# Kernel tuning notes

Hardware: AMD Instinct MI355X
Metric: run time of the kernel (lower is better)

## Reference

```python
import jax, jax.numpy as jnp
import numpy as np

D_MODEL = 768; N_LAYERS = 4; SOC_WINDOW = 10
D_INNER = 2 * D_MODEL; D_STATE = 16; DT_RANK = D_MODEL // 16; D_CONV = 4
EPS = 1e-5
B, T = 4, 1024


def setup_inputs() -> dict:
    key = jax.random.key(0)
    ks = jax.random.split(key, 10)
    w = lambda k, s, sc=0.02: jax.random.normal(k, s, jnp.float32) * sc
    return {
        "x": jax.random.normal(ks[0], (B, T, 2 + SOC_WINDOW), jnp.float32),
        "inp_w": w(ks[1], (D_MODEL, 2 + SOC_WINDOW)),
        "inp_b": jnp.zeros((D_MODEL,), jnp.float32),
        "in_proj_w": w(ks[2], (N_LAYERS, 2 * D_INNER, D_MODEL)),
        "conv_w": w(ks[3], (N_LAYERS, D_INNER, D_CONV), 0.1),
        "conv_b": jnp.zeros((N_LAYERS, D_INNER), jnp.float32),
        "x_proj_w": w(ks[4], (N_LAYERS, DT_RANK + 2 * D_STATE, D_INNER)),
        "dt_proj_w": w(ks[5], (N_LAYERS, D_INNER, DT_RANK), 0.05),
        "dt_proj_b": w(ks[6], (N_LAYERS, D_INNER), 0.5),
        "A_log": jnp.tile(jnp.log(jnp.arange(1.0, D_STATE + 1.0, dtype=jnp.float32)), (N_LAYERS, D_INNER, 1)),
        "D_skip": jnp.ones((N_LAYERS, D_INNER), jnp.float32),
        "out_proj_w": w(ks[7], (N_LAYERS, D_MODEL, D_INNER)),
        "ln_w": jnp.ones((N_LAYERS, D_MODEL), jnp.float32),
        "norm_w": jnp.ones((D_MODEL,), jnp.float32),
        "head_w": w(ks[8], (1, D_MODEL)),
        "head_b": jnp.zeros((1,), jnp.float32),
    }


def _rmsnorm(x, w):
    return x * jax.lax.rsqrt(jnp.mean(x * x, axis=-1, keepdims=True) + EPS) * w


def _mamba_block(x, in_w, cw, cb, xp_w, dtw, dtb, A_log, Dsk, out_w):
    Bsz = x.shape[0]
    xz = jnp.einsum('btd,ed->bte', x, in_w)            # (B,T,2*D_INNER)
    xx, z = jnp.split(xz, 2, axis=-1)
    # causal depthwise conv1d (pad left d_conv-1, truncate to T)
    xc = jax.lax.conv_general_dilated(
        jnp.swapaxes(xx, 1, 2), cw[:, None, :], (1,), [(D_CONV - 1, 0)],
        feature_group_count=D_INNER, dimension_numbers=('NCH', 'OIH', 'NCH'))
    xx = jax.nn.silu(jnp.swapaxes(xc + cb[None, :, None], 1, 2))  # (B,T,D_INNER)
    dbc = jnp.einsum('btd,ed->bte', xx, xp_w)          # (B,T,dt_rank+2*N)
    delta = jax.nn.softplus(jnp.einsum('btr,dr->btd', dbc[..., :DT_RANK], dtw) + dtb)
    Bm = dbc[..., DT_RANK:DT_RANK + D_STATE]           # (B,T,N)
    Cm = dbc[..., DT_RANK + D_STATE:]                  # (B,T,N)
    A = -jnp.exp(A_log)                                # (D_INNER,N)

    def step(h, inp):
        d_t, x_t, b_t, c_t = inp                       # (B,Din),(B,Din),(B,N),(B,N)
        h = jnp.exp(d_t[..., None] * A) * h + (d_t * x_t)[..., None] * b_t[:, None, :]
        return h, jnp.einsum('bdn,bn->bd', h, c_t)

    h0 = jnp.zeros((Bsz, D_INNER, D_STATE), x.dtype)
    _, ys = jax.lax.scan(step, h0, (jnp.moveaxis(delta, 1, 0), jnp.moveaxis(xx, 1, 0),
                                    jnp.moveaxis(Bm, 1, 0), jnp.moveaxis(Cm, 1, 0)))
    y = jnp.moveaxis(ys, 0, 1) + Dsk * xx
    y = y * jax.nn.silu(z)
    return jnp.einsum('bte,de->btd', y, out_w)


def reference(x, inp_w, inp_b, in_proj_w, conv_w, conv_b, x_proj_w, dt_proj_w, dt_proj_b,
              A_log, D_skip, out_proj_w, ln_w, norm_w, head_w, head_b):
    h = jnp.einsum('btf,df->btd', x, inp_w) + inp_b
    for l in range(N_LAYERS):
        h = h + _mamba_block(_rmsnorm(h, ln_w[l]), in_proj_w[l], conv_w[l], conv_b[l],
                             x_proj_w[l], dt_proj_w[l], dt_proj_b[l], A_log[l],
                             D_skip[l], out_proj_w[l])
    h = _rmsnorm(h, norm_w)
    y = jnp.einsum('btd,od->bto', h, head_w) + head_b
    return y[..., 0]
```

## Files before the change

### kernel.cpp

```cpp
#include <hip/hip_runtime.h>
#include <stdint.h>

#define D_MODEL   768
#define D_INNER   1536
#define D_STATE   16
#define DT_RANK   48
#define NB        4
#define TSEQ      1024
#define NTOK      4096
#define EPS       1e-5f
#define CHUNK     32
#define NCHUNK    32
#define XP_N      128

typedef __bf16 bf16;
typedef __bf16 bf16x8 __attribute__((ext_vector_type(8)));
typedef float  floatx4 __attribute__((ext_vector_type(4)));

__device__ __forceinline__ float silu_f(float v)     { return v / (1.f + __expf(-v)); }
__device__ __forceinline__ float softplus_f(float v) { return v > 20.f ? v : __logf(1.f + __expf(v)); }

__device__ __forceinline__ void async_ld16(const void* g, void* l) {
  __builtin_amdgcn_global_load_lds((__attribute__((address_space(1))) uint32_t*)g,
                                   (__attribute__((address_space(3))) uint32_t*)l, 16, 0, 0);
}

__global__ __launch_bounds__(256) void prep_k(const float* __restrict__ win, const float* __restrict__ wout,
                                              bf16* __restrict__ bin, bf16* __restrict__ bout) {
  const int i = blockIdx.x * 256 + threadIdx.x;
  const int NIN = 4 * 3072 * 768;
  if (i < NIN) bin[i] = (bf16)win[i];
  else         bout[i - NIN] = (bf16)wout[i - NIN];
}

__global__ __launch_bounds__(256) void prep_xp_k(const float* __restrict__ w, bf16* __restrict__ wb) {
  const int i = blockIdx.x * 256 + threadIdx.x;
  const int k = i % 1536;
  const int r = (i / 1536) % XP_N;
  const int l = i / (1536 * XP_N);
  wb[i] = (r < 80) ? (bf16)w[((size_t)l * 80 + r) * 1536 + k] : (bf16)0.f;
}

__global__ __launch_bounds__(256) void input_proj_k(const float* __restrict__ x, const float* __restrict__ w,
                                                    const float* __restrict__ bvec, float* __restrict__ h) {
  const int idx = blockIdx.x * 256 + threadIdx.x;
  const int d = idx % D_MODEL;
  const int t = idx / D_MODEL;
  float acc = bvec[d];
  #pragma unroll
  for (int f = 0; f < 12; ++f) acc = fmaf(x[t * 12 + f], w[d * 12 + f], acc);
  h[idx] = acc;
}

__global__ __launch_bounds__(256) void rmsnorm_k(const float* __restrict__ h, const float* __restrict__ lnw,
                                                 bf16* __restrict__ xn) {
  const int t = blockIdx.x;
  const float* __restrict__ hr = h + (size_t)t * D_MODEL;
  float v[3];
  float ss = 0.f;
  #pragma unroll
  for (int i = 0; i < 3; ++i) { v[i] = hr[threadIdx.x + i * 256]; ss = fmaf(v[i], v[i], ss); }
  #pragma unroll
  for (int o = 32; o > 0; o >>= 1) ss += __shfl_down(ss, o, 64);
  __shared__ float red[4];
  if ((threadIdx.x & 63) == 0) red[threadIdx.x >> 6] = ss;
  __syncthreads();
  const float tot = red[0] + red[1] + red[2] + red[3];
  const float rs = rsqrtf(tot / (float)D_MODEL + EPS);
  #pragma unroll
  for (int i = 0; i < 3; ++i) {
    const int d = threadIdx.x + i * 256;
    xn[(size_t)t * D_MODEL + d] = (bf16)(v[i] * rs * lnw[d]);
  }
}

template <int MODE>
__global__ __launch_bounds__(256) void gemm_bt(const bf16* __restrict__ A, const bf16* __restrict__ B,
                                               void* __restrict__ Cv, const int N, const int K, const int kLen) {
  alignas(16) __shared__ bf16 As[128 * 32];
  alignas(16) __shared__ bf16 Bs[128 * 32];
  const int tid = threadIdx.x;
  const int lane = tid & 63;
  const int wid = tid >> 6;
  const int wm = wid & 1, wn = wid >> 1;
  const int m0 = blockIdx.x * 128, n0 = blockIdx.y * 128;
  const int kOff = blockIdx.z * kLen;

  floatx4 acc[4][4];
  #pragma unroll
  for (int i = 0; i < 4; ++i)
    #pragma unroll
    for (int j = 0; j < 4; ++j) acc[i][j] = (floatx4){0.f, 0.f, 0.f, 0.f};

  const int srow = lane >> 2;
  const int skp  = (lane & 3) * 8;
  const int fr = lane & 15;
  const int fk = (lane >> 4) * 8;

  for (int k0 = 0; k0 < kLen; k0 += 32) {
    __syncthreads();
    #pragma unroll
    for (int i = 0; i < 2; ++i) {
      const int seg = wid * 2 + i;
      const int row = seg * 16 + srow;
      async_ld16(A + (size_t)(m0 + row) * K + kOff + k0 + skp, (char*)As + seg * 1024);
      async_ld16(B + (size_t)(n0 + row) * K + kOff + k0 + skp, (char*)Bs + seg * 1024);
    }
    __syncthreads();
    bf16x8 a[4], b[4];
    #pragma unroll
    for (int t = 0; t < 4; ++t) {
      a[t] = *(const bf16x8*)&As[(wm * 64 + t * 16 + fr) * 32 + fk];
      b[t] = *(const bf16x8*)&Bs[(wn * 64 + t * 16 + fr) * 32 + fk];
    }
    #pragma unroll
    for (int i = 0; i < 4; ++i)
      #pragma unroll
      for (int j = 0; j < 4; ++j)
        acc[i][j] = __builtin_amdgcn_mfma_f32_16x16x32_bf16(a[i], b[j], acc[i][j], 0, 0, 0);
  }

  const int quad = lane >> 4, col = lane & 15;
  #pragma unroll
  for (int i = 0; i < 4; ++i)
    #pragma unroll
    for (int j = 0; j < 4; ++j) {
      const int gm0 = m0 + wm * 64 + i * 16 + quad * 4;
      const int gn  = n0 + wn * 64 + j * 16 + col;
      #pragma unroll
      for (int r = 0; r < 4; ++r) {
        const size_t off = (size_t)(gm0 + r) * N + gn;
        const float v = acc[i][j][r];
        if (MODE == 0)      ((float*)Cv)[off] = v;
        else if (MODE == 1) ((bf16*)Cv)[off] = (bf16)v;
        else                atomicAdd(&((float*)Cv)[off], v);
      }
    }
}

__global__ __launch_bounds__(256) void conv_silu_k(const bf16* __restrict__ xz, const float* __restrict__ cw,
                                                   const float* __restrict__ cb, bf16* __restrict__ xxb) {
  const int idx = blockIdx.x * 256 + threadIdx.x;
  const int d = idx % D_INNER;
  const int bt = idx / D_INNER;
  const int t = bt & (TSEQ - 1);
  float acc = cb[d];
  #pragma unroll
  for (int j = 0; j < 4; ++j) {
    const int tt = t - 3 + j;
    if (tt >= 0) acc = fmaf((float)xz[(size_t)(bt - 3 + j) * (2 * D_INNER) + d], cw[d * 4 + j], acc);
  }
  xxb[idx] = (bf16)silu_f(acc);
}

__global__ __launch_bounds__(256) void scan_p1_k(const bf16* __restrict__ xxb, const float* __restrict__ dbc,
                                                 const float* __restrict__ dtw, const float* __restrict__ dtb,
                                                 const float* __restrict__ Alog,
                                                 float* __restrict__ P, float* __restrict__ S) {
  const int c = blockIdx.x;
  const int d = blockIdx.y * 256 + threadIdx.x;
  const int b = blockIdx.z;
  float w[DT_RANK];
  #pragma unroll
  for (int k = 0; k < DT_RANK; k += 4) {
    const float4 t4 = *(const float4*)&dtw[(size_t)d * DT_RANK + k];
    w[k] = t4.x; w[k + 1] = t4.y; w[k + 2] = t4.z; w[k + 3] = t4.w;
  }
  const float bias = dtb[d];
  float A[16], Sv[16], Pv[16];
  #pragma unroll
  for (int n = 0; n < 16; ++n) {
    A[n] = -__expf(Alog[(size_t)d * 16 + n]);
    Sv[n] = 0.f; Pv[n] = 1.f;
  }
  const int bt0 = b * TSEQ + c * CHUNK;
  for (int tt = 0; tt < CHUNK; ++tt) {
    const size_t bt = bt0 + tt;
    const float* __restrict__ db = dbc + bt * XP_N;
    float dacc = bias;
    #pragma unroll
    for (int k = 0; k < DT_RANK; ++k) dacc = fmaf(db[k], w[k], dacc);
    const float du  = softplus_f(dacc);
    const float xv  = (float)xxb[bt * D_INNER + d];
    const float dux = du * xv;
    const float* __restrict__ Bp = db + DT_RANK;
    #pragma unroll
    for (int n = 0; n < 16; ++n) {
      const float e = __expf(du * A[n]);
      Sv[n] = fmaf(e, Sv[n], dux * Bp[n]);
      Pv[n] *= e;
    }
  }
  const size_t base = ((size_t)(b * NCHUNK + c) * 16) * D_INNER + d;
  #pragma unroll
  for (int n = 0; n < 16; ++n) {
    P[base + (size_t)n * D_INNER] = Pv[n];
    S[base + (size_t)n * D_INNER] = Sv[n];
  }
}

__global__ __launch_bounds__(256) void scan_fold_k(const float* __restrict__ P, float* __restrict__ S) {
  const int idx = blockIdx.x * 256 + threadIdx.x;
  const int d = idx % D_INNER;
  const int bn = idx / D_INNER;
  const int n = bn & 15;
  const int b = bn >> 4;
  float H = 0.f;
  #pragma unroll 4
  for (int c = 0; c < NCHUNK; ++c) {
    const size_t off = ((size_t)((b * NCHUNK + c) * 16 + n)) * D_INNER + d;
    const float Pv = P[off], Sv = S[off];
    S[off] = H;
    H = fmaf(Pv, H, Sv);
  }
}

__global__ __launch_bounds__(256) void scan_p3_k(const bf16* __restrict__ xxb, const float* __restrict__ dbc,
                                                 const float* __restrict__ dtw, const float* __restrict__ dtb,
                                                 const float* __restrict__ Alog,
                                                 const float* __restrict__ Hin,
                                                 const bf16* __restrict__ xz, const float* __restrict__ Dsk,
                                                 bf16* __restrict__ yg) {
  const int c = blockIdx.x;
  const int d = blockIdx.y * 256 + threadIdx.x;
  const int b = blockIdx.z;
  float w[DT_RANK];
  #pragma unroll
  for (int k = 0; k < DT_RANK; k += 4) {
    const float4 t4 = *(const float4*)&dtw[(size_t)d * DT_RANK + k];
    w[k] = t4.x; w[k + 1] = t4.y; w[k + 2] = t4.z; w[k + 3] = t4.w;
  }
  const float bias = dtb[d];
  const size_t hbase = ((size_t)(b * NCHUNK + c) * 16) * D_INNER + d;
  float A[16], H[16];
  #pragma unroll
  for (int n = 0; n < 16; ++n) {
    A[n] = -__expf(Alog[(size_t)d * 16 + n]);
    H[n] = Hin[hbase + (size_t)n * D_INNER];
  }
  const float dsk = Dsk[d];
  const int bt0 = b * TSEQ + c * CHUNK;
  for (int tt = 0; tt < CHUNK; ++tt) {
    const size_t bt = bt0 + tt;
    const float* __restrict__ db = dbc + bt * XP_N;
    float dacc = bias;
    #pragma unroll
    for (int k = 0; k < DT_RANK; ++k) dacc = fmaf(db[k], w[k], dacc);
    const float du  = softplus_f(dacc);
    const float xv  = (float)xxb[bt * D_INNER + d];
    const float dux = du * xv;
    const float* __restrict__ Bp = db + DT_RANK;
    const float* __restrict__ Cp = db + DT_RANK + 16;
    float y = 0.f;
    #pragma unroll
    for (int n = 0; n < 16; ++n) {
      const float e = __expf(du * A[n]);
      H[n] = fmaf(e, H[n], dux * Bp[n]);
      y = fmaf(H[n], Cp[n], y);
    }
    const float z = (float)xz[bt * (2 * D_INNER) + D_INNER + d];
    yg[bt * D_INNER + d] = (bf16)((y + dsk * xv) * silu_f(z));
  }
}

__global__ __launch_bounds__(256) void final_k(const float* __restrict__ h, const float* __restrict__ nw,
                                               const float* __restrict__ hw, const float* __restrict__ hb,
                                               float* __restrict__ out) {
  const int t = blockIdx.x;
  const float* __restrict__ hr = h + (size_t)t * D_MODEL;
  float ss = 0.f, dt_ = 0.f;
  #pragma unroll
  for (int i = 0; i < 3; ++i) {
    const int d = threadIdx.x + i * 256;
    const float v = hr[d];
    ss  = fmaf(v, v, ss);
    dt_ = fmaf(v, nw[d] * hw[d], dt_);
  }
  #pragma unroll
  for (int o = 32; o > 0; o >>= 1) { ss += __shfl_down(ss, o, 64); dt_ += __shfl_down(dt_, o, 64); }
  __shared__ float r0[4], r1[4];
  if ((threadIdx.x & 63) == 0) { r0[threadIdx.x >> 6] = ss; r1[threadIdx.x >> 6] = dt_; }
  __syncthreads();
  if (threadIdx.x == 0) {
    const float sst = r0[0] + r0[1] + r0[2] + r0[3];
    const float dtt = r1[0] + r1[1] + r1[2] + r1[3];
    out[t] = dtt * rsqrtf(sst / (float)D_MODEL + EPS) + hb[0];
  }
}

extern "C" void kernel_launch(void* const* d_in, const int* in_sizes, int n_in,
                              void* d_out, int out_size, void* d_ws, size_t ws_size,
                              hipStream_t stream) {
  (void)in_sizes; (void)n_in; (void)out_size; (void)ws_size;
  const float* x     = (const float*)d_in[0];
  const float* inpw  = (const float*)d_in[1];
  const float* inpb  = (const float*)d_in[2];
  const float* inprj = (const float*)d_in[3];
  const float* convw = (const float*)d_in[4];
  const float* convb = (const float*)d_in[5];
  const float* xprjw = (const float*)d_in[6];
  const float* dtw   = (const float*)d_in[7];
  const float* dtb   = (const float*)d_in[8];
  const float* alog  = (const float*)d_in[9];
  const float* dskip = (const float*)d_in[10];
  const float* outw  = (const float*)d_in[11];
  const float* lnw   = (const float*)d_in[12];
  const float* normw = (const float*)d_in[13];
  const float* headw = (const float*)d_in[14];
  const float* headb = (const float*)d_in[15];
  float* out = (float*)d_out;

  char* p = (char*)d_ws;
  auto take = [&](size_t bytes) { char* q = p; p += (bytes + 255) & ~(size_t)255; return q; };
  bf16*  wbin  = (bf16*) take((size_t)4 * 3072 * 768 * 2);
  bf16*  wbout = (bf16*) take((size_t)4 * 768 * 1536 * 2);
  bf16*  wbxp  = (bf16*) take((size_t)4 * XP_N * 1536 * 2);
  float* h     = (float*)take((size_t)NTOK * D_MODEL * 4);
  bf16*  xn    = (bf16*) take((size_t)NTOK * D_MODEL * 2);
  bf16*  xzb   = (bf16*) take((size_t)NTOK * 2 * D_INNER * 2);
  bf16*  xxb   = (bf16*) take((size_t)NTOK * D_INNER * 2);
  float* dbc   = (float*)take((size_t)NTOK * XP_N * 4);
  float* Pb    = (float*)take((size_t)NB * NCHUNK * 16 * D_INNER * 4);
  float* Sb    = (float*)take((size_t)NB * NCHUNK * 16 * D_INNER * 4);
  bf16*  yg    = (bf16*) take((size_t)NTOK * D_INNER * 2);

  prep_k<<<55296, 256, 0, stream>>>(inprj, outw, wbin, wbout);
  prep_xp_k<<<4 * XP_N * 1536 / 256, 256, 0, stream>>>(xprjw, wbxp);
  input_proj_k<<<NTOK * D_MODEL / 256, 256, 0, stream>>>(x, inpw, inpb, h);

  for (int l = 0; l < 4; ++l) {
    rmsnorm_k<<<NTOK, 256, 0, stream>>>(h, lnw + l * D_MODEL, xn);
    gemm_bt<1><<<dim3(32, 24, 1), 256, 0, stream>>>(xn, wbin + (size_t)l * 3072 * 768, xzb, 3072, 768, 768);
    conv_silu_k<<<NTOK * D_INNER / 256, 256, 0, stream>>>(xzb, convw + l * D_INNER * 4, convb + l * D_INNER, xxb);
    hipMemsetAsync(dbc, 0, (size_t)NTOK * XP_N * 4, stream);
    gemm_bt<2><<<dim3(32, 1, 4), 256, 0, stream>>>(xxb, wbxp + (size_t)l * XP_N * 1536, dbc, XP_N, 1536, 384);
    scan_p1_k<<<dim3(NCHUNK, 6, NB), 256, 0, stream>>>(xxb, dbc, dtw + (size_t)l * D_INNER * DT_RANK,
                                                       dtb + l * D_INNER, alog + (size_t)l * D_INNER * 16, Pb, Sb);
    scan_fold_k<<<NB * 16 * D_INNER / 256, 256, 0, stream>>>(Pb, Sb);
    scan_p3_k<<<dim3(NCHUNK, 6, NB), 256, 0, stream>>>(xxb, dbc, dtw + (size_t)l * D_INNER * DT_RANK,
                                                       dtb + l * D_INNER, alog + (size_t)l * D_INNER * 16,
                                                       Sb, xzb, dskip + l * D_INNER, yg);
    gemm_bt<2><<<dim3(32, 6, 2), 256, 0, stream>>>(yg, wbout + (size_t)l * 768 * 1536, h, 768, 1536, 768);
  }

  final_k<<<NTOK, 256, 0, stream>>>(h, normw, headw, headb, out);
}
```

Measured before the change: 968.9 us.

## Cache delta, derive chunk decay from delta sums, and use exp powers for A

The first scan pass now writes the softplus delta and a per-chunk sum of delta. The third pass reads delta back instead of recomputing the 48-wide dt projection. The fold kernel rebuilds each chunk's decay product as exp(A·sum delta), so the per-state P buffer is dropped. When A_log matches log(1..16), which is checked at runtime with a general fallback, the 16 exps per step become one exp plus repeated multiplies. The cost is a new full-size fp32 delta buffer written and re-read every layer, plus a small rounding change from computing the powers by repeated multiplication.

```diff
diff --git a/kernel.cpp b/kernel.cpp
--- a/kernel.cpp
+++ b/kernel.cpp
@@ -156,7 +156,8 @@
 __global__ __launch_bounds__(256) void scan_p1_k(const bf16* __restrict__ xxb, const float* __restrict__ dbc,
                                                  const float* __restrict__ dtw, const float* __restrict__ dtb,
                                                  const float* __restrict__ Alog,
-                                                 float* __restrict__ P, float* __restrict__ S) {
+                                                 float* __restrict__ S, float* __restrict__ su,
+                                                 float* __restrict__ delta) {
   const int c = blockIdx.x;
   const int d = blockIdx.y * 256 + threadIdx.x;
   const int b = blockIdx.z;
@@ -167,99 +168,137 @@
     w[k] = t4.x; w[k + 1] = t4.y; w[k + 2] = t4.z; w[k + 3] = t4.w;
   }
   const float bias = dtb[d];
-  float A[16], Sv[16], Pv[16];
+  float A[16], Sv[16];
+  bool fast = true;
   #pragma unroll
   for (int n = 0; n < 16; ++n) {
     A[n] = -__expf(Alog[(size_t)d * 16 + n]);
-    Sv[n] = 0.f; Pv[n] = 1.f;
-  }
+    fast = fast && (__builtin_fabsf(A[n] + (float)(n + 1)) < 1e-3f);
+    Sv[n] = 0.f;
+  }
+  float sus = 0.f;
   const int bt0 = b * TSEQ + c * CHUNK;
-  for (int tt = 0; tt < CHUNK; ++tt) {
-    const size_t bt = bt0 + tt;
-    const float* __restrict__ db = dbc + bt * XP_N;
-    float dacc = bias;
-    #pragma unroll
-    for (int k = 0; k < DT_RANK; ++k) dacc = fmaf(db[k], w[k], dacc);
-    const float du  = softplus_f(dacc);
-    const float xv  = (float)xxb[bt * D_INNER + d];
-    const float dux = du * xv;
-    const float* __restrict__ Bp = db + DT_RANK;
-    #pragma unroll
-    for (int n = 0; n < 16; ++n) {
-      const float e = __expf(du * A[n]);
-      Sv[n] = fmaf(e, Sv[n], dux * Bp[n]);
-      Pv[n] *= e;
+  if (fast) {
+    for (int tt = 0; tt < CHUNK; ++tt) {
+      const size_t bt = bt0 + tt;
+      const float* __restrict__ db = dbc + bt * XP_N;
+      float dacc = bias;
+      #pragma unroll
+      for (int k = 0; k < DT_RANK; ++k) dacc = fmaf(db[k], w[k], dacc);
+      const float du = softplus_f(dacc);
+      delta[bt * D_INNER + d] = du;
+      sus += du;
+      const float xv  = (float)xxb[bt * D_INNER + d];
+      const float dux = du * xv;
+      const float* __restrict__ Bp = db + DT_RANK;
+      const float r = __expf(-du);
+      float e = r;
+      #pragma unroll
+      for (int n = 0; n < 16; ++n) {
+        Sv[n] = fmaf(e, Sv[n], dux * Bp[n]);
+        e *= r;
+      }
+    }
+  } else {
+    for (int tt = 0; tt < CHUNK; ++tt) {
+      const size_t bt = bt0 + tt;
+      const float* __restrict__ db = dbc + bt * XP_N;
+      float dacc = bias;
+      #pragma unroll
+      for (int k = 0; k < DT_RANK; ++k) dacc = fmaf(db[k], w[k], dacc);
+      const float du = softplus_f(dacc);
+      delta[bt * D_INNER + d] = du;
+      sus += du;
+      const float xv  = (float)xxb[bt * D_INNER + d];
+      const float dux = du * xv;
+      const float* __restrict__ Bp = db + DT_RANK;
+      #pragma unroll
+      for (int n = 0; n < 16; ++n)
+        Sv[n] = fmaf(__expf(du * A[n]), Sv[n], dux * Bp[n]);
     }
   }
   const size_t base = ((size_t)(b * NCHUNK + c) * 16) * D_INNER + d;
   #pragma unroll
-  for (int n = 0; n < 16; ++n) {
-    P[base + (size_t)n * D_INNER] = Pv[n];
-    S[base + (size_t)n * D_INNER] = Sv[n];
-  }
-}
-
-__global__ __launch_bounds__(256) void scan_fold_k(const float* __restrict__ P, float* __restrict__ S) {
+  for (int n = 0; n < 16; ++n) S[base + (size_t)n * D_INNER] = Sv[n];
+  su[(size_t)(b * NCHUNK + c) * D_INNER + d] = sus;
+}
+
+__global__ __launch_bounds__(256) void scan_fold_k(const float* __restrict__ Alog, const float* __restrict__ su,
+                                                   float* __restrict__ S) {
   const int idx = blockIdx.x * 256 + threadIdx.x;
   const int d = idx % D_INNER;
   const int bn = idx / D_INNER;
   const int n = bn & 15;
   const int b = bn >> 4;
+  const float A = -__expf(Alog[(size_t)d * 16 + n]);
   float H = 0.f;
   #pragma unroll 4
   for (int c = 0; c < NCHUNK; ++c) {
     const size_t off = ((size_t)((b * NCHUNK + c) * 16 + n)) * D_INNER + d;
-    const float Pv = P[off], Sv = S[off];
+    const float Pv = __expf(A * su[(size_t)(b * NCHUNK + c) * D_INNER + d]);
+    const float Sv = S[off];
     S[off] = H;
     H = fmaf(Pv, H, Sv);
   }
 }
 
 __global__ __launch_bounds__(256) void scan_p3_k(const bf16* __restrict__ xxb, const float* __restrict__ dbc,
-                                                 const float* __restrict__ dtw, const float* __restrict__ dtb,
-                                                 const float* __restrict__ Alog,
+                                                 const float* __restrict__ delta, const float* __restrict__ Alog,
                                                  const float* __restrict__ Hin,
                                                  const bf16* __restrict__ xz, const float* __restrict__ Dsk,
                                                  bf16* __restrict__ yg) {
   const int c = blockIdx.x;
   const int d = blockIdx.y * 256 + threadIdx.x;
   const int b = blockIdx.z;
-  float w[DT_RANK];
-  #pragma unroll
-  for (int k = 0; k < DT_RANK; k += 4) {
-    const float4 t4 = *(const float4*)&dtw[(size_t)d * DT_RANK + k];
-    w[k] = t4.x; w[k + 1] = t4.y; w[k + 2] = t4.z; w[k + 3] = t4.w;
-  }
-  const float bias = dtb[d];
   const size_t hbase = ((size_t)(b * NCHUNK + c) * 16) * D_INNER + d;
   float A[16], H[16];
+  bool fast = true;
   #pragma unroll
   for (int n = 0; n < 16; ++n) {
     A[n] = -__expf(Alog[(size_t)d * 16 + n]);
+    fast = fast && (__builtin_fabsf(A[n] + (float)(n + 1)) < 1e-3f);
     H[n] = Hin[hbase + (size_t)n * D_INNER];
   }
   const float dsk = Dsk[d];
   const int bt0 = b * TSEQ + c * CHUNK;
-  for (int tt = 0; tt < CHUNK; ++tt) {
-    const size_t bt = bt0 + tt;
-    const float* __restrict__ db = dbc + bt * XP_N;
-    float dacc = bias;
-    #pragma unroll
-    for (int k = 0; k < DT_RANK; ++k) dacc = fmaf(db[k], w[k], dacc);
-    const float du  = softplus_f(dacc);
-    const float xv  = (float)xxb[bt * D_INNER + d];
-    const float dux = du * xv;
-    const float* __restrict__ Bp = db + DT_RANK;
-    const float* __restrict__ Cp = db + DT_RANK + 16;
-    float y = 0.f;
-    #pragma unroll
-    for (int n = 0; n < 16; ++n) {
-      const float e = __expf(du * A[n]);
-      H[n] = fmaf(e, H[n], dux * Bp[n]);
-      y = fmaf(H[n], Cp[n], y);
-    }
-    const float z = (float)xz[bt * (2 * D_INNER) + D_INNER + d];
-    yg[bt * D_INNER + d] = (bf16)((y + dsk * xv) * silu_f(z));
+  if (fast) {
+    for (int tt = 0; tt < CHUNK; ++tt) {
+      const size_t bt = bt0 + tt;
+      const float du  = delta[bt * D_INNER + d];
+      const float xv  = (float)xxb[bt * D_INNER + d];
+      const float dux = du * xv;
+      const float* __restrict__ db = dbc + bt * XP_N;
+      const float* __restrict__ Bp = db + DT_RANK;
+      const float* __restrict__ Cp = db + DT_RANK + 16;
+      const float r = __expf(-du);
+      float e = r, y = 0.f;
+      #pragma unroll
+      for (int n = 0; n < 16; ++n) {
+        H[n] = fmaf(e, H[n], dux * Bp[n]);
+        y = fmaf(H[n], Cp[n], y);
+        e *= r;
+      }
+      const float z = (float)xz[bt * (2 * D_INNER) + D_INNER + d];
+      yg[bt * D_INNER + d] = (bf16)((y + dsk * xv) * silu_f(z));
+    }
+  } else {
+    for (int tt = 0; tt < CHUNK; ++tt) {
+      const size_t bt = bt0 + tt;
+      const float du  = delta[bt * D_INNER + d];
+      const float xv  = (float)xxb[bt * D_INNER + d];
+      const float dux = du * xv;
+      const float* __restrict__ db = dbc + bt * XP_N;
+      const float* __restrict__ Bp = db + DT_RANK;
+      const float* __restrict__ Cp = db + DT_RANK + 16;
+      float y = 0.f;
+      #pragma unroll
+      for (int n = 0; n < 16; ++n) {
+        H[n] = fmaf(__expf(du * A[n]), H[n], dux * Bp[n]);
+        y = fmaf(H[n], Cp[n], y);
+      }
+      const float z = (float)xz[bt * (2 * D_INNER) + D_INNER + d];
+      yg[bt * D_INNER + d] = (bf16)((y + dsk * xv) * silu_f(z));
+    }
   }
 }
 
@@ -320,8 +359,9 @@
   bf16*  xzb   = (bf16*) take((size_t)NTOK * 2 * D_INNER * 2);
   bf16*  xxb   = (bf16*) take((size_t)NTOK * D_INNER * 2);
   float* dbc   = (float*)take((size_t)NTOK * XP_N * 4);
-  float* Pb    = (float*)take((size_t)NB * NCHUNK * 16 * D_INNER * 4);
+  float* dlt   = (float*)take((size_t)NTOK * D_INNER * 4);
   float* Sb    = (float*)take((size_t)NB * NCHUNK * 16 * D_INNER * 4);
+  float* su    = (float*)take((size_t)NB * NCHUNK * D_INNER * 4);
   bf16*  yg    = (bf16*) take((size_t)NTOK * D_INNER * 2);
 
   prep_k<<<55296, 256, 0, stream>>>(inprj, outw, wbin, wbout);
@@ -335,10 +375,10 @@
     hipMemsetAsync(dbc, 0, (size_t)NTOK * XP_N * 4, stream);
     gemm_bt<2><<<dim3(32, 1, 4), 256, 0, stream>>>(xxb, wbxp + (size_t)l * XP_N * 1536, dbc, XP_N, 1536, 384);
     scan_p1_k<<<dim3(NCHUNK, 6, NB), 256, 0, stream>>>(xxb, dbc, dtw + (size_t)l * D_INNER * DT_RANK,
-                                                       dtb + l * D_INNER, alog + (size_t)l * D_INNER * 16, Pb, Sb);
-    scan_fold_k<<<NB * 16 * D_INNER / 256, 256, 0, stream>>>(Pb, Sb);
-    scan_p3_k<<<dim3(NCHUNK, 6, NB), 256, 0, stream>>>(xxb, dbc, dtw + (size_t)l * D_INNER * DT_RANK,
                                                        dtb + l * D_INNER, alog + (size_t)l * D_INNER * 16,
+                                                       Sb, su, dlt);
+    scan_fold_k<<<NB * 16 * D_INNER / 256, 256, 0, stream>>>(alog + (size_t)l * D_INNER * 16, su, Sb);
+    scan_p3_k<<<dim3(NCHUNK, 6, NB), 256, 0, stream>>>(xxb, dbc, dlt, alog + (size_t)l * D_INNER * 16,
                                                        Sb, xzb, dskip + l * D_INNER, yg);
     gemm_bt<2><<<dim3(32, 6, 2), 256, 0, stream>>>(yg, wbout + (size_t)l * 768 * 1536, h, 768, 1536, 768);
   }
```

Measured after the change: 867.4 us. 10.5% less time.
